# Kernel optimization log

Hardware: AMD Instinct MI355X
Metric: run time of the kernel (lower is better)

## Reference

```python
import jax, jax.numpy as jnp
import numpy as np

D_MODEL = 128
NUM_HEADS = 8
HEAD_DIM = D_MODEL // NUM_HEADS
LN_EPS = 1e-5


def layernorm(x, gamma, beta):
    mu = jnp.mean(x, axis=-1, keepdims=True)
    var = jnp.mean(jnp.square(x - mu), axis=-1, keepdims=True)
    return (x - mu) * jax.lax.rsqrt(var + LN_EPS) * gamma + beta


def setup_inputs() -> dict:
    key = jax.random.key(0)
    ks = jax.random.split(key, 12)
    B, L, d = 16, 1024, D_MODEL
    scale = 1.0 / np.sqrt(d)
    edge_x = jax.random.normal(ks[0], (B, L, d), dtype=jnp.float32)
    # True entries are masked out (masked_fill with -inf)
    edge_mask = jax.random.randint(ks[1], (B, L, L), 0, 2).astype(jnp.bool_)
    in_proj_w = jax.random.normal(ks[2], (d, 3 * d), dtype=jnp.float32) * scale  # fused QKV
    in_proj_b = jnp.zeros((3 * d,), dtype=jnp.float32)
    w1 = jax.random.normal(ks[3], (d, d), dtype=jnp.float32) * scale
    b1 = jnp.zeros((d,), dtype=jnp.float32)
    w2 = jax.random.normal(ks[4], (d, d), dtype=jnp.float32) * scale
    b2 = jnp.zeros((d,), dtype=jnp.float32)
    g1 = jnp.ones((d,), dtype=jnp.float32)
    beta1 = jnp.zeros((d,), dtype=jnp.float32)
    g2 = jnp.ones((d,), dtype=jnp.float32)
    beta2 = jnp.zeros((d,), dtype=jnp.float32)
    return {"edge_x": edge_x, "edge_mask": edge_mask, "in_proj_w": in_proj_w,
            "in_proj_b": in_proj_b, "w1": w1, "b1": b1, "w2": w2, "b2": b2,
            "g1": g1, "beta1": beta1, "g2": g2, "beta2": beta2}


def reference(edge_x, edge_mask, in_proj_w, in_proj_b, w1, b1, w2, b2, g1, beta1, g2, beta2):
    B, L, d = edge_x.shape
    H, hd = NUM_HEADS, HEAD_DIM
    scaling = float(hd) ** -0.5
    # fused QKV projection
    qkv = edge_x @ in_proj_w + in_proj_b              # [B, L, 3d]
    q, k, v = jnp.split(qkv, 3, axis=-1)
    q = q.reshape(B, L, H, hd).transpose(0, 2, 1, 3)  # [B, H, L, hd]
    k = k.reshape(B, L, H, hd).transpose(0, 2, 1, 3)
    v = v.reshape(B, L, H, hd).transpose(0, 2, 1, 3)
    scores = jnp.einsum('bhqd,bhkd->bhqk', q, k) * scaling  # [B, H, L, L]
    scores = jnp.where(edge_mask[:, None, :, :], -jnp.inf, scores)
    attn = jax.nn.softmax(scores, axis=-1)
    ctx = jnp.einsum('bhqk,bhkd->bhqd', attn, v)      # [B, H, L, hd]
    ctx = ctx.transpose(0, 2, 1, 3).reshape(B, L, d)
    # residual + LayerNorm
    x = layernorm(edge_x + ctx, g1, beta1)
    # FFN (relu), residual + LayerNorm (dropout=0 in eval mode)
    ff = jax.nn.relu(x @ w1 + b1) @ w2 + b2
    x = layernorm(x + ff, g2, beta2)
    return x
```

## Files before the change

### kernel.cpp

```cpp
#include <hip/hip_runtime.h>
#include <cstdint>

#define NROWS 16384
#define ARRE ((size_t)NROWS * 128)

typedef short short8 __attribute__((ext_vector_type(8)));
typedef float f32x4  __attribute__((ext_vector_type(4)));
typedef float f32x16 __attribute__((ext_vector_type(16)));

static __device__ __forceinline__ unsigned short f2bf(float f) {
    union { float f; uint32_t u; } v; v.f = f;
    uint32_t r = v.u + 0x7fffu + ((v.u >> 16) & 1u);
    return (unsigned short)(r >> 16);
}

static __device__ __forceinline__ uint32_t cvt_pk_bf16(float lo, float hi) {
    uint32_t r;
    asm("v_cvt_pk_bf16_f32 %0, %1, %2" : "=v"(r) : "v"(lo), "v"(hi));
    return r;
}

__global__ void k_detect(const uint32_t* __restrict__ m, int* __restrict__ flag) {
    if (threadIdx.x == 0) {
        int f = 0;
        for (int i = 0; i < 256; ++i) f |= (m[i] > 1u) ? 1 : 0;
        *flag = f;
    }
}

__global__ void k_castw(const float* __restrict__ wqkv, const float* __restrict__ w1,
                        const float* __restrict__ w2, unsigned short* __restrict__ wT)
{
    const int e = blockIdx.x * 256 + threadIdx.x;
    if (e < 49152) {
        const int n = e >> 7, k = e & 127;
        wT[e] = f2bf(wqkv[k * 384 + n]);
    } else if (e < 65536) {
        const int i = e - 49152, n = i >> 7, k = i & 127;
        wT[e] = f2bf(w1[k * 128 + n]);
    } else if (e < 81920) {
        const int i = e - 65536, n = i >> 7, k = i & 127;
        wT[e] = f2bf(w2[k * 128 + n]);
    }
}

template<int NF, int MODE>
__global__ __launch_bounds__(256, 2) void k_mm(const float* __restrict__ Xf,
        const unsigned short* __restrict__ Wt, const float* __restrict__ bias,
        unsigned short* __restrict__ out)
{
    __shared__ char smem[16384 + NF * 4096];
    char* const sX = smem;
    char* const sW = smem + 16384;
    const int t = threadIdx.x;
    const int w = t >> 6, l = t & 63;
    const int l4 = l >> 4, l15 = l & 15;
    const int r0 = blockIdx.x * 64;
    const int c0 = blockIdx.y * (NF * 16);

    #pragma unroll
    for (int i = 0; i < 4; ++i) {
        const int c = t + 256 * i;
        const int row = c >> 4, slot = c & 15;
        const float4* src = (const float4*)(Xf + (size_t)(r0 + row) * 128 + slot * 8);
        float4 f0 = src[0], f1 = src[1];
        uint4 v;
        v.x = cvt_pk_bf16(f0.x, f0.y);
        v.y = cvt_pk_bf16(f0.z, f0.w);
        v.z = cvt_pk_bf16(f1.x, f1.y);
        v.w = cvt_pk_bf16(f1.z, f1.w);
        *(uint4*)(sX + row * 256 + ((slot ^ (row & 15)) << 4)) = v;
    }
    #pragma unroll
    for (int i = 0; i < NF; ++i) {
        const int c = t + 256 * i;
        const int col = c >> 4, slot = c & 15;
        uint4 v = *(const uint4*)(Wt + (size_t)(c0 + col) * 128 + slot * 8);
        *(uint4*)(sW + col * 256 + ((slot ^ (col & 15)) << 4)) = v;
    }
    __syncthreads();

    short8 aF[4];
    #pragma unroll
    for (int kk = 0; kk < 4; ++kk)
        aF[kk] = *(const short8*)(sX + (w * 16 + l15) * 256 + (((kk * 4 + l4) ^ l15) << 4));

    f32x4 acc[NF];
    #pragma unroll
    for (int nf = 0; nf < NF; ++nf) acc[nf] = f32x4{0.f, 0.f, 0.f, 0.f};
    #pragma unroll
    for (int nf = 0; nf < NF; ++nf) {
        #pragma unroll
        for (int kk = 0; kk < 4; ++kk) {
            short8 bF = *(const short8*)(sW + (nf * 16 + l15) * 256 + (((kk * 4 + l4) ^ l15) << 4));
            acc[nf] = __builtin_amdgcn_mfma_f32_16x16x32_bf16(bF, aF[kk], acc[nf], 0, 0, 0);
        }
    }

    const float scl = (MODE == 0 && blockIdx.y == 0) ? 0.25f : 1.0f;
    const int row = r0 + w * 16 + l15;
    #pragma unroll
    for (int nf = 0; nf < NF; ++nf) {
        const int cb = nf * 16 + l4 * 4;
        float4 bv = *(const float4*)(bias + c0 + cb);
        float v0 = acc[nf][0] + bv.x, v1 = acc[nf][1] + bv.y;
        float v2 = acc[nf][2] + bv.z, v3 = acc[nf][3] + bv.w;
        if (MODE == 1) {
            v0 = fmaxf(v0, 0.f); v1 = fmaxf(v1, 0.f);
            v2 = fmaxf(v2, 0.f); v3 = fmaxf(v3, 0.f);
        }
        v0 *= scl; v1 *= scl; v2 *= scl; v3 *= scl;
        uint2 pk;
        pk.x = cvt_pk_bf16(v0, v1);
        pk.y = cvt_pk_bf16(v2, v3);
        size_t o;
        if (MODE == 0) o = (size_t)blockIdx.y * ARRE + (size_t)row * 128 + cb;
        else           o = (size_t)row * 128 + c0 + cb;
        *(uint2*)(out + o) = pk;
    }
}

__global__ __launch_bounds__(256, 2) void k_mm2(const unsigned short* __restrict__ h1,
        const unsigned short* __restrict__ w2t, const float* __restrict__ b2,
        const float* __restrict__ x1, const float* __restrict__ g2,
        const float* __restrict__ be2, float* __restrict__ out)
{
    __shared__ char smem[16384 + 32768];
    char* const sX = smem;
    char* const sW = smem + 16384;
    const int t = threadIdx.x;
    const int w = t >> 6, l = t & 63;
    const int l4 = l >> 4, l15 = l & 15;
    const int r0 = blockIdx.x * 64;

    #pragma unroll
    for (int i = 0; i < 4; ++i) {
        const int c = t + 256 * i;
        const int row = c >> 4, slot = c & 15;
        uint4 v = *(const uint4*)(h1 + (size_t)(r0 + row) * 128 + slot * 8);
        *(uint4*)(sX + row * 256 + ((slot ^ (row & 15)) << 4)) = v;
    }
    #pragma unroll
    for (int i = 0; i < 8; ++i) {
        const int c = t + 256 * i;
        const int col = c >> 4, slot = c & 15;
        uint4 v = *(const uint4*)(w2t + (size_t)col * 128 + slot * 8);
        *(uint4*)(sW + col * 256 + ((slot ^ (col & 15)) << 4)) = v;
    }
    __syncthreads();

    short8 aF[4];
    #pragma unroll
    for (int kk = 0; kk < 4; ++kk)
        aF[kk] = *(const short8*)(sX + (w * 16 + l15) * 256 + (((kk * 4 + l4) ^ l15) << 4));

    f32x4 acc[8];
    #pragma unroll
    for (int nf = 0; nf < 8; ++nf) acc[nf] = f32x4{0.f, 0.f, 0.f, 0.f};
    #pragma unroll
    for (int nf = 0; nf < 8; ++nf) {
        #pragma unroll
        for (int kk = 0; kk < 4; ++kk) {
            short8 bF = *(const short8*)(sW + (nf * 16 + l15) * 256 + (((kk * 4 + l4) ^ l15) << 4));
            acc[nf] = __builtin_amdgcn_mfma_f32_16x16x32_bf16(bF, aF[kk], acc[nf], 0, 0, 0);
        }
    }

    const int row = r0 + w * 16 + l15;
    float y[8][4];
    float s = 0.f;
    #pragma unroll
    for (int nf = 0; nf < 8; ++nf) {
        const int cb = nf * 16 + l4 * 4;
        float4 bv = *(const float4*)(b2 + cb);
        float4 xv = *(const float4*)(x1 + (size_t)row * 128 + cb);
        y[nf][0] = acc[nf][0] + bv.x + xv.x;
        y[nf][1] = acc[nf][1] + bv.y + xv.y;
        y[nf][2] = acc[nf][2] + bv.z + xv.z;
        y[nf][3] = acc[nf][3] + bv.w + xv.w;
        s += y[nf][0] + y[nf][1] + y[nf][2] + y[nf][3];
    }
    s += __shfl_xor(s, 16); s += __shfl_xor(s, 32);
    const float mu = s * (1.f / 128.f);
    float vv = 0.f;
    #pragma unroll
    for (int nf = 0; nf < 8; ++nf) {
        #pragma unroll
        for (int reg = 0; reg < 4; ++reg) { float d = y[nf][reg] - mu; vv += d * d; }
    }
    vv += __shfl_xor(vv, 16); vv += __shfl_xor(vv, 32);
    const float rs = rsqrtf(vv * (1.f / 128.f) + 1e-5f);
    #pragma unroll
    for (int nf = 0; nf < 8; ++nf) {
        const int cb = nf * 16 + l4 * 4;
        float4 gv = *(const float4*)(g2 + cb);
        float4 ev = *(const float4*)(be2 + cb);
        float4 o;
        o.x = (y[nf][0] - mu) * rs * gv.x + ev.x;
        o.y = (y[nf][1] - mu) * rs * gv.y + ev.y;
        o.z = (y[nf][2] - mu) * rs * gv.z + ev.z;
        o.w = (y[nf][3] - mu) * rs * gv.w + ev.w;
        *(float4*)(out + (size_t)row * 128 + cb) = o;
    }
}

__global__ __launch_bounds__(512, 2) void k_attn(
        const unsigned short* __restrict__ qb,
        const unsigned short* __restrict__ kb,
        const unsigned short* __restrict__ vbp,
        const void* __restrict__ maskp, const int* __restrict__ flag,
        const float* __restrict__ x, const float* __restrict__ g1,
        const float* __restrict__ be1, float* __restrict__ x1)
{
    __shared__ alignas(16) char smem[39072];
    char*          const sK = smem;
    char*          const sV = smem + 8192;
    char*          const sP = smem + 17440;
    unsigned char* const sM = (unsigned char*)(smem + 37920);
    float*         const sS = (float*)(smem + 38048);

    const int t  = threadIdx.x;
    const int w  = t >> 6;
    const int l  = t & 63;
    const int b  = blockIdx.y;
    const int q0 = blockIdx.x * 32;
    const int q   = l & 31;
    const int hi  = l >> 5;
    const int l4  = l >> 4;
    const int l15 = l & 15;
    const int bytemask = *flag;

    short8 qf;
    {
        const size_t qrow = (size_t)(b * 1024 + q0 + q) * 128;
        qf = *(const short8*)(qb + qrow + w * 16 + hi * 8);
    }
    float m = -INFINITY, ls = 0.f;
    f32x4 ac0 = {0,0,0,0}, ac1 = {0,0,0,0};
    const f32x16 z16 = {};
    float* const sSw = sS + w * 32;
    char*  const Pw  = sP + w * 2560;

    const uint8_t* m8  = (const uint8_t*)maskp;
    const int*     m32 = (const int*)maskp;

    for (int kt = 0; kt < 32; ++kt) {
        const int k0 = kt * 32;
        __syncthreads();
        {
            const int row = t >> 4, slot = t & 15;
            const size_t src = (size_t)(b * 1024 + k0 + row) * 128 + slot * 8;
            uint4 kv = *(const uint4*)(kb + src);
            *(uint4*)(sK + row * 256 + ((slot ^ (row & 15)) << 4)) = kv;
            uint4 vv = *(const uint4*)(vbp + src);
            unsigned short* dh = (unsigned short*)(sV + (slot >> 1) * 1156);
            uint32_t* dst = (uint32_t*)(dh + row * 18 + (slot & 1) * 8);
            dst[0] = vv.x; dst[1] = vv.y; dst[2] = vv.z; dst[3] = vv.w;
        }
        if (t < 128) {
            const int mq = t >> 2, g = t & 3;
            const size_t moff = ((size_t)b << 20) + (size_t)(q0 + mq) * 1024
                              + (size_t)(k0 + g * 8);
            unsigned int bits = 0;
            if (bytemask) {
                uint64_t v = *(const uint64_t*)(m8 + moff);
                #pragma unroll
                for (int j = 0; j < 8; ++j)
                    bits |= ((((v >> (8 * j)) & 0xffull) == 0ull) ? 1u : 0u) << j;
            } else {
                const int4* p = (const int4*)(m32 + moff);
                int4 va = p[0], vc = p[1];
                bits = (va.x==0?1u:0u) | (va.y==0?2u:0u) | (va.z==0?4u:0u) | (va.w==0?8u:0u)
                     | (vc.x==0?16u:0u) | (vc.y==0?32u:0u) | (vc.z==0?64u:0u) | (vc.w==0?128u:0u);
            }
            sM[mq * 4 + g] = (unsigned char)bits;
        }
        __syncthreads();

        const uint32_t mk = *(const uint32_t*)(sM + q * 4);
        const uint32_t mks = mk >> (4 * hi);

        short8 kf = *(const short8*)(sK + q * 256 + ((((w << 1) + hi) ^ (q & 15)) << 4));
        f32x16 sc = __builtin_amdgcn_mfma_f32_32x32x16_bf16(kf, qf, z16, 0, 0, 0);
        float sm = sc[0];
        #pragma unroll
        for (int r = 1; r < 16; ++r) sm = fmaxf(sm, sc[r]);
        sm = fmaxf(sm, __shfl_xor(sm, 32));
        if (__any(sm > m + 8.f)) {
            float nm = fmaxf(m, sm);
            float s  = __expf(m - nm);
            m = nm; ls *= s;
            sSw[q] = s;
            float4 s0v = *(float4*)&sSw[l4 * 4];
            float4 s1v = *(float4*)&sSw[l4 * 4 + 16];
            ac0[0] *= s0v.x; ac0[1] *= s0v.y; ac0[2] *= s0v.z; ac0[3] *= s0v.w;
            ac1[0] *= s1v.x; ac1[1] *= s1v.y; ac1[2] *= s1v.z; ac1[3] *= s1v.w;
        }
        float p[16]; float lsum = 0.f;
        #pragma unroll
        for (int r = 0; r < 16; ++r) {
            const int c = (r & 3) + 8 * (r >> 2);
            float pv = __expf(sc[r] - m);
            pv = ((mks >> c) & 1u) ? pv : 0.f;
            lsum += pv; p[r] = pv;
        }
        ls += lsum;
        #pragma unroll
        for (int g = 0; g < 4; ++g) {
            uint2 pk;
            pk.x = cvt_pk_bf16(p[4*g+0], p[4*g+1]);
            pk.y = cvt_pk_bf16(p[4*g+2], p[4*g+3]);
            *(uint2*)(Pw + q * 80 + (8 * g + 4 * hi) * 2) = pk;
        }
        short8 pa0 = *(const short8*)(Pw + l15 * 80 + l4 * 16);
        short8 pa1 = *(const short8*)(Pw + (l15 + 16) * 80 + l4 * 16);
        const unsigned short* sVh = (const unsigned short*)(sV + w * 1156);
        short8 vf;
        #pragma unroll
        for (int j = 0; j < 8; ++j)
            vf[j] = (short)sVh[(l4 * 8 + j) * 18 + l15];
        ac0 = __builtin_amdgcn_mfma_f32_16x16x32_bf16(pa0, vf, ac0, 0, 0, 0);
        ac1 = __builtin_amdgcn_mfma_f32_16x16x32_bf16(pa1, vf, ac1, 0, 0, 0);
    }

    __syncthreads();
    float* const sC = (float*)smem;
    {
        float lt  = ls + __shfl_xor(ls, 32);
        float inv = 1.f / lt;
        sSw[q] = inv;
        float4 i0 = *(float4*)&sSw[l4 * 4];
        float4 i1 = *(float4*)&sSw[l4 * 4 + 16];
        const int cc = w * 16 + l15;
        sC[(l4 * 4 + 0) * 132 + cc]  = ac0[0] * i0.x;
        sC[(l4 * 4 + 1) * 132 + cc]  = ac0[1] * i0.y;
        sC[(l4 * 4 + 2) * 132 + cc]  = ac0[2] * i0.z;
        sC[(l4 * 4 + 3) * 132 + cc]  = ac0[3] * i0.w;
        sC[(l4 * 4 + 16) * 132 + cc] = ac1[0] * i1.x;
        sC[(l4 * 4 + 17) * 132 + cc] = ac1[1] * i1.y;
        sC[(l4 * 4 + 18) * 132 + cc] = ac1[2] * i1.z;
        sC[(l4 * 4 + 19) * 132 + cc] = ac1[3] * i1.w;
    }
    __syncthreads();

    {
        const int row = t >> 4;
        const int c0  = (t & 15) * 8;
        const size_t grow = (size_t)(b * 1024 + q0 + row);
        const float4* xp = (const float4*)(x + grow * 128 + c0);
        const float4* cp = (const float4*)(sC + row * 132 + c0);
        float y[8];
        float s = 0.f;
        #pragma unroll
        for (int j = 0; j < 2; ++j) {
            float4 xv = xp[j], cv = cp[j];
            y[4*j+0] = xv.x + cv.x; y[4*j+1] = xv.y + cv.y;
            y[4*j+2] = xv.z + cv.z; y[4*j+3] = xv.w + cv.w;
            s += y[4*j+0] + y[4*j+1] + y[4*j+2] + y[4*j+3];
        }
        s += __shfl_xor(s, 1); s += __shfl_xor(s, 2);
        s += __shfl_xor(s, 4); s += __shfl_xor(s, 8);
        const float mu = s * (1.f / 128.f);
        float vv = 0.f;
        #pragma unroll
        for (int e = 0; e < 8; ++e) { float d = y[e] - mu; vv += d * d; }
        vv += __shfl_xor(vv, 1); vv += __shfl_xor(vv, 2);
        vv += __shfl_xor(vv, 4); vv += __shfl_xor(vv, 8);
        const float rs = rsqrtf(vv * (1.f / 128.f) + 1e-5f);
        #pragma unroll
        for (int j = 0; j < 2; ++j) {
            float4 gv = *(const float4*)(g1 + c0 + 4 * j);
            float4 bv = *(const float4*)(be1 + c0 + 4 * j);
            float4 o;
            o.x = (y[4*j+0] - mu) * rs * gv.x + bv.x;
            o.y = (y[4*j+1] - mu) * rs * gv.y + bv.y;
            o.z = (y[4*j+2] - mu) * rs * gv.z + bv.z;
            o.w = (y[4*j+3] - mu) * rs * gv.w + bv.w;
            *(float4*)(x1 + grow * 128 + c0 + 4 * j) = o;
        }
    }
}

extern "C" void kernel_launch(void* const* d_in, const int* in_sizes, int n_in,
                              void* d_out, int out_size, void* d_ws, size_t ws_size,
                              hipStream_t stream)
{
    const float* x    = (const float*)d_in[0];
    const void*  mask = d_in[1];
    const float* wqkv = (const float*)d_in[2];
    const float* bqkv = (const float*)d_in[3];
    const float* w1   = (const float*)d_in[4];
    const float* b1   = (const float*)d_in[5];
    const float* w2   = (const float*)d_in[6];
    const float* b2   = (const float*)d_in[7];
    const float* g1   = (const float*)d_in[8];
    const float* be1  = (const float*)d_in[9];
    const float* g2   = (const float*)d_in[10];
    const float* be2  = (const float*)d_in[11];
    float* out = (float*)d_out;

    char* base = (char*)d_ws;
    int* flag = (int*)base;
    unsigned short* qb  = (unsigned short*)(base + 256);
    unsigned short* kb  = qb + ARRE;
    unsigned short* vb  = kb + ARRE;
    float* x1           = (float*)(base + 256 + (size_t)12 * 1024 * 1024);
    unsigned short* wT  = (unsigned short*)(base + 256 + (size_t)20 * 1024 * 1024);
    unsigned short* h1b = qb;

    k_detect<<<1, 64, 0, stream>>>((const uint32_t*)mask, flag);
    k_castw<<<320, 256, 0, stream>>>(wqkv, w1, w2, wT);
    k_mm<8, 0><<<dim3(256, 3), 256, 0, stream>>>(x, wT, bqkv, qb);
    k_attn<<<dim3(32, 16), 512, 0, stream>>>(qb, kb, vb, mask, flag, x, g1, be1, x1);
    k_mm<4, 1><<<dim3(256, 2), 256, 0, stream>>>(x1, wT + 49152, b1, h1b);
    k_mm2<<<256, 256, 0, stream>>>(h1b, wT + 65536, b2, x1, g2, be2, out);
}
```

Measured before the change: 196.9 us.

## Fuse FFN GEMMs, merge mask detect into weight cast, transpose V in LDS

```diff
diff --git a/kernel.cpp b/kernel.cpp
--- a/kernel.cpp
+++ b/kernel.cpp
@@ -20,17 +20,24 @@
     return r;
 }
 
-__global__ void k_detect(const uint32_t* __restrict__ m, int* __restrict__ flag) {
-    if (threadIdx.x == 0) {
-        int f = 0;
-        for (int i = 0; i < 256; ++i) f |= (m[i] > 1u) ? 1 : 0;
-        *flag = f;
-    }
+static __device__ __forceinline__ float v_exp2(float x) {
+    float r;
+    asm("v_exp_f32 %0, %1" : "=v"(r) : "v"(x));
+    return r;
 }
 
 __global__ void k_castw(const float* __restrict__ wqkv, const float* __restrict__ w1,
-                        const float* __restrict__ w2, unsigned short* __restrict__ wT)
+                        const float* __restrict__ w2, unsigned short* __restrict__ wT,
+                        const uint32_t* __restrict__ mask, int* __restrict__ flag)
 {
+    if (blockIdx.x == 320) {
+        if (threadIdx.x == 0) {
+            int f = 0;
+            for (int i = 0; i < 256; ++i) f |= (mask[i] > 1u) ? 1 : 0;
+            *flag = f;
+        }
+        return;
+    }
     const int e = blockIdx.x * 256 + threadIdx.x;
     if (e < 49152) {
         const int n = e >> 7, k = e & 127;
@@ -97,7 +104,7 @@
         }
     }
 
-    const float scl = (MODE == 0 && blockIdx.y == 0) ? 0.25f : 1.0f;
+    const float scl = (MODE == 0 && blockIdx.y == 0) ? 0.36067376022224085f : 1.0f;
     const int row = r0 + w * 16 + l15;
     #pragma unroll
     for (int nf = 0; nf < NF; ++nf) {
@@ -120,12 +127,13 @@
     }
 }
 
-__global__ __launch_bounds__(256, 2) void k_mm2(const unsigned short* __restrict__ h1,
+__global__ __launch_bounds__(256, 2) void k_ffn(const float* __restrict__ x1,
+        const unsigned short* __restrict__ w1t, const float* __restrict__ b1,
         const unsigned short* __restrict__ w2t, const float* __restrict__ b2,
-        const float* __restrict__ x1, const float* __restrict__ g2,
-        const float* __restrict__ be2, float* __restrict__ out)
+        const float* __restrict__ g2, const float* __restrict__ be2,
+        float* __restrict__ out)
 {
-    __shared__ char smem[16384 + 32768];
+    __shared__ char smem[49152];
     char* const sX = smem;
     char* const sW = smem + 16384;
     const int t = threadIdx.x;
@@ -137,8 +145,59 @@
     for (int i = 0; i < 4; ++i) {
         const int c = t + 256 * i;
         const int row = c >> 4, slot = c & 15;
-        uint4 v = *(const uint4*)(h1 + (size_t)(r0 + row) * 128 + slot * 8);
+        const float4* src = (const float4*)(x1 + (size_t)(r0 + row) * 128 + slot * 8);
+        float4 f0 = src[0], f1 = src[1];
+        uint4 v;
+        v.x = cvt_pk_bf16(f0.x, f0.y);
+        v.y = cvt_pk_bf16(f0.z, f0.w);
+        v.z = cvt_pk_bf16(f1.x, f1.y);
+        v.w = cvt_pk_bf16(f1.z, f1.w);
         *(uint4*)(sX + row * 256 + ((slot ^ (row & 15)) << 4)) = v;
+    }
+    #pragma unroll
+    for (int i = 0; i < 8; ++i) {
+        const int c = t + 256 * i;
+        const int col = c >> 4, slot = c & 15;
+        uint4 v = *(const uint4*)(w1t + (size_t)col * 128 + slot * 8);
+        *(uint4*)(sW + col * 256 + ((slot ^ (col & 15)) << 4)) = v;
+    }
+    __syncthreads();
+
+    short8 aF[4];
+    #pragma unroll
+    for (int kk = 0; kk < 4; ++kk)
+        aF[kk] = *(const short8*)(sX + (w * 16 + l15) * 256 + (((kk * 4 + l4) ^ l15) << 4));
+
+    f32x4 acc[8];
+    #pragma unroll
+    for (int nf = 0; nf < 8; ++nf) acc[nf] = f32x4{0.f, 0.f, 0.f, 0.f};
+    #pragma unroll
+    for (int nf = 0; nf < 8; ++nf) {
+        #pragma unroll
+        for (int kk = 0; kk < 4; ++kk) {
+            short8 bF = *(const short8*)(sW + (nf * 16 + l15) * 256 + (((kk * 4 + l4) ^ l15) << 4));
+            acc[nf] = __builtin_amdgcn_mfma_f32_16x16x32_bf16(bF, aF[kk], acc[nf], 0, 0, 0);
+        }
+    }
+    __syncthreads();
+
+    {
+        const int hrow = w * 16 + l15;
+        #pragma unroll
+        for (int nf = 0; nf < 8; ++nf) {
+            const int cb = nf * 16 + l4 * 4;
+            float4 bv = *(const float4*)(b1 + cb);
+            float v0 = fmaxf(acc[nf][0] + bv.x, 0.f);
+            float v1 = fmaxf(acc[nf][1] + bv.y, 0.f);
+            float v2 = fmaxf(acc[nf][2] + bv.z, 0.f);
+            float v3 = fmaxf(acc[nf][3] + bv.w, 0.f);
+            uint2 pk;
+            pk.x = cvt_pk_bf16(v0, v1);
+            pk.y = cvt_pk_bf16(v2, v3);
+            const int slot = (2 * nf) + (l4 >> 1);
+            const int off  = (l4 & 1) * 8;
+            *(uint2*)(sX + hrow * 256 + ((slot ^ (hrow & 15)) << 4) + off) = pk;
+        }
     }
     #pragma unroll
     for (int i = 0; i < 8; ++i) {
@@ -149,20 +208,20 @@
     }
     __syncthreads();
 
-    short8 aF[4];
+    short8 aG[4];
     #pragma unroll
     for (int kk = 0; kk < 4; ++kk)
-        aF[kk] = *(const short8*)(sX + (w * 16 + l15) * 256 + (((kk * 4 + l4) ^ l15) << 4));
-
-    f32x4 acc[8];
-    #pragma unroll
-    for (int nf = 0; nf < 8; ++nf) acc[nf] = f32x4{0.f, 0.f, 0.f, 0.f};
+        aG[kk] = *(const short8*)(sX + (w * 16 + l15) * 256 + (((kk * 4 + l4) ^ l15) << 4));
+
+    f32x4 acc2[8];
+    #pragma unroll
+    for (int nf = 0; nf < 8; ++nf) acc2[nf] = f32x4{0.f, 0.f, 0.f, 0.f};
     #pragma unroll
     for (int nf = 0; nf < 8; ++nf) {
         #pragma unroll
         for (int kk = 0; kk < 4; ++kk) {
             short8 bF = *(const short8*)(sW + (nf * 16 + l15) * 256 + (((kk * 4 + l4) ^ l15) << 4));
-            acc[nf] = __builtin_amdgcn_mfma_f32_16x16x32_bf16(bF, aF[kk], acc[nf], 0, 0, 0);
+            acc2[nf] = __builtin_amdgcn_mfma_f32_16x16x32_bf16(bF, aG[kk], acc2[nf], 0, 0, 0);
         }
     }
 
@@ -174,10 +233,10 @@
         const int cb = nf * 16 + l4 * 4;
         float4 bv = *(const float4*)(b2 + cb);
         float4 xv = *(const float4*)(x1 + (size_t)row * 128 + cb);
-        y[nf][0] = acc[nf][0] + bv.x + xv.x;
-        y[nf][1] = acc[nf][1] + bv.y + xv.y;
-        y[nf][2] = acc[nf][2] + bv.z + xv.z;
-        y[nf][3] = acc[nf][3] + bv.w + xv.w;
+        y[nf][0] = acc2[nf][0] + bv.x + xv.x;
+        y[nf][1] = acc2[nf][1] + bv.y + xv.y;
+        y[nf][2] = acc2[nf][2] + bv.z + xv.z;
+        y[nf][3] = acc2[nf][3] + bv.w + xv.w;
         s += y[nf][0] + y[nf][1] + y[nf][2] + y[nf][3];
     }
     s += __shfl_xor(s, 16); s += __shfl_xor(s, 32);
@@ -212,18 +271,19 @@
         const float* __restrict__ x, const float* __restrict__ g1,
         const float* __restrict__ be1, float* __restrict__ x1)
 {
-    __shared__ alignas(16) char smem[39072];
-    char*          const sK = smem;
-    char*          const sV = smem + 8192;
-    char*          const sP = smem + 17440;
-    unsigned char* const sM = (unsigned char*)(smem + 37920);
-    float*         const sS = (float*)(smem + 38048);
+    __shared__ alignas(16) char smem[41216];
+    char*          const sK  = smem;
+    char*          const sVT = smem + 9216;
+    char*          const sP  = smem + 19584;
+    unsigned char* const sM  = (unsigned char*)(smem + 40064);
+    float*         const sS  = (float*)(smem + 40192);
 
     const int t  = threadIdx.x;
     const int w  = t >> 6;
     const int l  = t & 63;
-    const int b  = blockIdx.y;
-    const int q0 = blockIdx.x * 32;
+    const int bid = blockIdx.x;
+    const int b  = ((bid & 7) << 1) | ((bid >> 3) >> 5);
+    const int q0 = ((bid >> 3) & 31) * 32;
     const int q   = l & 31;
     const int hi  = l >> 5;
     const int l4  = l >> 4;
@@ -251,11 +311,18 @@
             const int row = t >> 4, slot = t & 15;
             const size_t src = (size_t)(b * 1024 + k0 + row) * 128 + slot * 8;
             uint4 kv = *(const uint4*)(kb + src);
-            *(uint4*)(sK + row * 256 + ((slot ^ (row & 15)) << 4)) = kv;
+            *(uint4*)(sK + row * 288 + ((slot ^ (row & 15)) << 4)) = kv;
             uint4 vv = *(const uint4*)(vbp + src);
-            unsigned short* dh = (unsigned short*)(sV + (slot >> 1) * 1156);
-            uint32_t* dst = (uint32_t*)(dh + row * 18 + (slot & 1) * 8);
-            dst[0] = vv.x; dst[1] = vv.y; dst[2] = vv.z; dst[3] = vv.w;
+            char* vt = sVT + (slot >> 1) * 1296 + (slot & 1) * 640 + row * 2;
+            const uint32_t w0 = vv.x, w1 = vv.y, w2 = vv.z, w3 = vv.w;
+            *(unsigned short*)(vt + 0 * 80) = (unsigned short)(w0);
+            *(unsigned short*)(vt + 1 * 80) = (unsigned short)(w0 >> 16);
+            *(unsigned short*)(vt + 2 * 80) = (unsigned short)(w1);
+            *(unsigned short*)(vt + 3 * 80) = (unsigned short)(w1 >> 16);
+            *(unsigned short*)(vt + 4 * 80) = (unsigned short)(w2);
+            *(unsigned short*)(vt + 5 * 80) = (unsigned short)(w2 >> 16);
+            *(unsigned short*)(vt + 6 * 80) = (unsigned short)(w3);
+            *(unsigned short*)(vt + 7 * 80) = (unsigned short)(w3 >> 16);
         }
         if (t < 128) {
             const int mq = t >> 2, g = t & 3;
@@ -280,7 +347,7 @@
         const uint32_t mk = *(const uint32_t*)(sM + q * 4);
         const uint32_t mks = mk >> (4 * hi);
 
-        short8 kf = *(const short8*)(sK + q * 256 + ((((w << 1) + hi) ^ (q & 15)) << 4));
+        short8 kf = *(const short8*)(sK + q * 288 + ((((w << 1) + hi) ^ (q & 15)) << 4));
         f32x16 sc = __builtin_amdgcn_mfma_f32_32x32x16_bf16(kf, qf, z16, 0, 0, 0);
         float sm = sc[0];
         #pragma unroll
@@ -288,7 +355,7 @@
         sm = fmaxf(sm, __shfl_xor(sm, 32));
         if (__any(sm > m + 8.f)) {
             float nm = fmaxf(m, sm);
-            float s  = __expf(m - nm);
+            float s  = v_exp2(m - nm);
             m = nm; ls *= s;
             sSw[q] = s;
             float4 s0v = *(float4*)&sSw[l4 * 4];
@@ -300,7 +367,7 @@
         #pragma unroll
         for (int r = 0; r < 16; ++r) {
             const int c = (r & 3) + 8 * (r >> 2);
-            float pv = __expf(sc[r] - m);
+            float pv = v_exp2(sc[r] - m);
             pv = ((mks >> c) & 1u) ? pv : 0.f;
             lsum += pv; p[r] = pv;
         }
@@ -314,11 +381,7 @@
         }
         short8 pa0 = *(const short8*)(Pw + l15 * 80 + l4 * 16);
         short8 pa1 = *(const short8*)(Pw + (l15 + 16) * 80 + l4 * 16);
-        const unsigned short* sVh = (const unsigned short*)(sV + w * 1156);
-        short8 vf;
-        #pragma unroll
-        for (int j = 0; j < 8; ++j)
-            vf[j] = (short)sVh[(l4 * 8 + j) * 18 + l15];
+        short8 vf  = *(const short8*)(sVT + w * 1296 + l15 * 80 + l4 * 16);
         ac0 = __builtin_amdgcn_mfma_f32_16x16x32_bf16(pa0, vf, ac0, 0, 0, 0);
         ac1 = __builtin_amdgcn_mfma_f32_16x16x32_bf16(pa1, vf, ac1, 0, 0, 0);
     }
@@ -406,12 +469,9 @@
     unsigned short* vb  = kb + ARRE;
     float* x1           = (float*)(base + 256 + (size_t)12 * 1024 * 1024);
     unsigned short* wT  = (unsigned short*)(base + 256 + (size_t)20 * 1024 * 1024);
-    unsigned short* h1b = qb;
-
-    k_detect<<<1, 64, 0, stream>>>((const uint32_t*)mask, flag);
-    k_castw<<<320, 256, 0, stream>>>(wqkv, w1, w2, wT);
+
+    k_castw<<<321, 256, 0, stream>>>(wqkv, w1, w2, wT, (const uint32_t*)mask, flag);
     k_mm<8, 0><<<dim3(256, 3), 256, 0, stream>>>(x, wT, bqkv, qb);
-    k_attn<<<dim3(32, 16), 512, 0, stream>>>(qb, kb, vb, mask, flag, x, g1, be1, x1);
-    k_mm<4, 1><<<dim3(256, 2), 256, 0, stream>>>(x1, wT + 49152, b1, h1b);
-    k_mm2<<<256, 256, 0, stream>>>(h1b, wT + 65536, b2, x1, g2, be2, out);
-}
+    k_attn<<<512, 512, 0, stream>>>(qb, kb, vb, mask, flag, x, g1, be1, x1);
+    k_ffn<<<256, 256, 0, stream>>>(x1, wT + 49152, b1, wT + 65536, b2, g2, be2, out);
+}
```

Measured after the change: 197.5 us. No clear change (+0.3%).
